# Performance work log

Measured on AMD Instinct MI355X. Metric: run time of the kernel, lower is better.

## Reference

```python
import jax, jax.numpy as jnp
import numpy as np

N_NODES = 10000
N_EDGES = 80000
OBS_DIMS = 128
HIDDEN = 1024
ACT_DIMS = 8
N_GRAPHS = 64


def setup_inputs() -> dict:
    key = jax.random.key(0)
    ks = jax.random.split(key, 8)
    x = jax.random.normal(ks[0], (N_NODES, OBS_DIMS), dtype=jnp.float32)
    edge_index = jax.random.randint(ks[1], (2, N_EDGES), 0, N_NODES, dtype=jnp.int64)
    batch = jnp.sort(jax.random.randint(ks[2], (N_NODES,), 0, N_GRAPHS, dtype=jnp.int64))
    # Glorot-style init for weights, zero bias (as in PyG GCNConv / Linear defaults)
    W1 = jax.random.normal(ks[3], (OBS_DIMS, HIDDEN), dtype=jnp.float32) * (1.0 / np.sqrt(OBS_DIMS))
    b1 = jnp.zeros((HIDDEN,), dtype=jnp.float32)
    W2 = jax.random.normal(ks[4], (HIDDEN, HIDDEN), dtype=jnp.float32) * (1.0 / np.sqrt(HIDDEN))
    b2 = jnp.zeros((HIDDEN,), dtype=jnp.float32)
    Wl = jax.random.normal(ks[5], (HIDDEN, ACT_DIMS), dtype=jnp.float32) * (1.0 / np.sqrt(HIDDEN))
    bl = jnp.zeros((ACT_DIMS,), dtype=jnp.float32)
    return {"x": x, "edge_index": edge_index, "batch": batch,
            "W1": W1, "b1": b1, "W2": W2, "b2": b2, "Wl": Wl, "bl": bl}


def _gcn_conv(x, src, dst, dinv, W, b, n):
    """PyG GCNConv: D^-1/2 (A+I) D^-1/2 X W + b (self-loops already in src/dst)."""
    h = x @ W                                   # [N, out]
    norm = (dinv[src] * dinv[dst])[:, None]      # [E+N, 1]
    msg = h[src] * norm                          # gather + scale
    out = jax.ops.segment_sum(msg, dst, num_segments=n)
    return out + b


def reference(x, edge_index, batch, W1, b1, W2, b2, Wl, bl):
    n = x.shape[0]
    loops = jnp.arange(n, dtype=edge_index.dtype)
    src = jnp.concatenate([edge_index[0], loops])  # add self-loops
    dst = jnp.concatenate([edge_index[1], loops])
    # degree (with self-loops) from destination column, as PyG does
    deg = jax.ops.segment_sum(jnp.ones_like(dst, dtype=x.dtype), dst, num_segments=n)
    dinv = jax.lax.rsqrt(jnp.maximum(deg, 1.0))

    h = jax.nn.relu(_gcn_conv(x, src, dst, dinv, W1, b1, n))
    h = _gcn_conv(h, src, dst, dinv, W2, b2, n)
    h = jnp.tanh(h @ Wl + bl)                    # [N, act_dims]

    # global_mean_pool over batch segment ids
    sums = jax.ops.segment_sum(h, batch, num_segments=N_GRAPHS)
    counts = jax.ops.segment_sum(jnp.ones((n, 1), h.dtype), batch, num_segments=N_GRAPHS)
    return sums / jnp.maximum(counts, 1.0)       # [N_GRAPHS, act_dims]
```

## Files before the change

kernel.cpp:

```cpp
#include <hip/hip_runtime.h>
#include <hip/hip_bf16.h>

#define NNODES 10000
#define NEDGES 80000
#define OBS    128
#define HID    1024
#define ACTD   8
#define NGR    64

typedef __bf16 bf16x8 __attribute__((ext_vector_type(8)));
typedef float  f32x4  __attribute__((ext_vector_type(4)));
typedef const __attribute__((address_space(1))) unsigned int gl_u32;
typedef __attribute__((address_space(3))) unsigned int lds_u32;

__device__ __forceinline__ ushort f2b(float f) {
    union { float f; unsigned int i; } v; v.f = f;
    unsigned int lsb = (v.i >> 16) & 1u;
    unsigned int r = v.i + 0x7fffu + lsb;
    return (ushort)(r >> 16);
}
__device__ __forceinline__ int cix(int v, int hi) {
    return v < 0 ? 0 : (v >= hi ? hi - 1 : v);
}

__global__ __launch_bounds__(256) void k_prep(const float* __restrict__ W1,
                                              const float* __restrict__ W2,
                                              const float* __restrict__ Wl,
                                              const float* __restrict__ b2,
                                              const float* __restrict__ bl,
                                              ushort* __restrict__ Wt1,
                                              ushort* __restrict__ M2bf,
                                              float* __restrict__ b2l,
                                              float* __restrict__ zacc,
                                              float* __restrict__ pool,
                                              float* __restrict__ cnt,
                                              int* __restrict__ ticket,
                                              int* __restrict__ degi) {
    int blk = blockIdx.x;
    if (blk >= 385) {
        int idx = (blk - 385) * 256 + threadIdx.x;
        if (idx < NNODES * ACTD) zacc[idx] = 0.0f;
        if (idx < NGR * ACTD) pool[idx] = 0.0f;
        if (idx < NGR) cnt[idx] = 0.0f;
        if (idx < NNODES) degi[idx] = 0;
        if (idx == 0) *ticket = 0;
        return;
    }
    if (blk < 128) {
        __shared__ float tile[32][33];
        int bx = (blk & 31) * 32, by = (blk >> 5) * 32;
        int tx = threadIdx.x & 31, ty = threadIdx.x >> 5;
        #pragma unroll
        for (int i = 0; i < 32; i += 8)
            tile[ty + i][tx] = W1[(size_t)(by + ty + i) * HID + bx + tx];
        __syncthreads();
        #pragma unroll
        for (int i = 0; i < 32; i += 8)
            Wt1[(size_t)(bx + ty + i) * OBS + by + tx] = f2b(tile[tx][ty + i]);
        return;
    }
    int wvid = ((blk - 128) * 256 + (int)threadIdx.x) >> 6;
    int lane = threadIdx.x & 63;
    if (wvid > HID) return;
    const float* row = (wvid == HID) ? b2 : (W2 + (size_t)wvid * HID);
    float acc[ACTD];
    #pragma unroll
    for (int j = 0; j < ACTD; ++j) acc[j] = 0.0f;
    for (int it = 0; it < HID / 64; ++it) {
        int k = it * 64 + lane;
        float w2v = row[k];
        float4 a = *(const float4*)(Wl + (size_t)k * ACTD);
        float4 b = *(const float4*)(Wl + (size_t)k * ACTD + 4);
        acc[0] += w2v * a.x; acc[1] += w2v * a.y; acc[2] += w2v * a.z; acc[3] += w2v * a.w;
        acc[4] += w2v * b.x; acc[5] += w2v * b.y; acc[6] += w2v * b.z; acc[7] += w2v * b.w;
    }
    #pragma unroll
    for (int off = 32; off > 0; off >>= 1)
        #pragma unroll
        for (int j = 0; j < ACTD; ++j)
            acc[j] += __shfl_down(acc[j], off);
    if (lane == 0) {
        if (wvid == HID) {
            #pragma unroll
            for (int j = 0; j < ACTD; ++j) b2l[j] = acc[j] + bl[j];
        } else {
            #pragma unroll
            for (int j = 0; j < ACTD; ++j) M2bf[wvid * ACTD + j] = f2b(acc[j]);
        }
    }
}

__global__ void k_count(const int* __restrict__ dst, int* degi, int e) {
    int i = blockIdx.x * 256 + threadIdx.x;
    if (i < e) atomicAdd(&degi[cix(dst[i], NNODES)], 1);
}

__global__ __launch_bounds__(1024) void k_scan(const int* __restrict__ degi,
                                               int* rowptr, int* cursor, float* dinv) {
    __shared__ int wsum[16];
    int t = threadIdx.x, lane = t & 63, w = t >> 6;
    int base = t * 10;
    int local[10];
    int s = 0;
    #pragma unroll
    for (int k = 0; k < 10; ++k) {
        int i = base + k;
        int v = 0;
        if (i < NNODES) {
            v = degi[i];
            dinv[i] = rsqrtf((float)(v + 1));
        }
        local[k] = s; s += v;
    }
    int sc = s;
    #pragma unroll
    for (int off = 1; off < 64; off <<= 1) {
        int u = __shfl_up(sc, off);
        if (lane >= off) sc += u;
    }
    if (lane == 63) wsum[w] = sc;
    __syncthreads();
    if (w == 0 && lane < 16) {
        int v = wsum[lane];
        #pragma unroll
        for (int off = 1; off < 16; off <<= 1) {
            int u = __shfl_up(v, off);
            if (lane >= off) v += u;
        }
        wsum[lane] = v;
    }
    __syncthreads();
    int excl = ((w == 0) ? 0 : wsum[w - 1]) + (sc - s);
    #pragma unroll
    for (int k = 0; k < 10; ++k) {
        int i = base + k;
        if (i < NNODES) { rowptr[i] = excl + local[k]; cursor[i] = excl + local[k]; }
    }
    if (t == 0) rowptr[NNODES] = wsum[15];
}

__global__ void k_fill(const int* __restrict__ src, const int* __restrict__ dst,
                       const float* __restrict__ dinv, int* cursor,
                       int2* __restrict__ epair, int e) {
    int i = blockIdx.x * 256 + threadIdx.x;
    if (i >= e) return;
    int s = cix(src[i], NNODES), d = cix(dst[i], NNODES);
    int pos = atomicAdd(&cursor[d], 1);
    epair[pos] = make_int2(s, __float_as_int(dinv[s] * dinv[d]));
}

__global__ void k_aggx(const float* __restrict__ x, const float* __restrict__ dinv,
                       const int* __restrict__ rowptr, const int2* __restrict__ epair,
                       ushort* __restrict__ aggbf, int n) {
    int wv = (blockIdx.x * 256 + threadIdx.x) >> 6;
    int lane = threadIdx.x & 63;
    if (wv >= n) return;
    int half = lane >> 5, li = lane & 31;
    float acc0 = 0.f, acc1 = 0.f, acc2 = 0.f, acc3 = 0.f;
    if (half == 0) {
        float d = dinv[wv], d2 = d * d;
        float4 sv = *((const float4*)(x + (size_t)wv * OBS) + li);
        acc0 = sv.x * d2; acc1 = sv.y * d2; acc2 = sv.z * d2; acc3 = sv.w * d2;
    }
    int e1 = rowptr[wv + 1];
    int e = rowptr[wv] + half;
    for (; e + 2 < e1; e += 4) {
        int2 p0 = epair[e], p1 = epair[e + 2];
        float c0 = __int_as_float(p0.y), c1 = __int_as_float(p1.y);
        float4 a = *((const float4*)(x + (size_t)p0.x * OBS) + li);
        float4 b = *((const float4*)(x + (size_t)p1.x * OBS) + li);
        acc0 += a.x * c0 + b.x * c1;
        acc1 += a.y * c0 + b.y * c1;
        acc2 += a.z * c0 + b.z * c1;
        acc3 += a.w * c0 + b.w * c1;
    }
    if (e < e1) {
        int2 p0 = epair[e];
        float c0 = __int_as_float(p0.y);
        float4 a = *((const float4*)(x + (size_t)p0.x * OBS) + li);
        acc0 += a.x * c0; acc1 += a.y * c0; acc2 += a.z * c0; acc3 += a.w * c0;
    }
    acc0 += __shfl_down(acc0, 32);
    acc1 += __shfl_down(acc1, 32);
    acc2 += __shfl_down(acc2, 32);
    acc3 += __shfl_down(acc3, 32);
    if (half == 0) {
        ushort4 o; o.x = f2b(acc0); o.y = f2b(acc1); o.z = f2b(acc2); o.w = f2b(acc3);
        *((ushort4*)(aggbf + (size_t)wv * OBS) + li) = o;
    }
}

__global__ __launch_bounds__(256) void k_gemm1_fused(const ushort* __restrict__ A,
                                                     const ushort* __restrict__ Bt,
                                                     const float* __restrict__ bias,
                                                     const ushort* __restrict__ M2bf,
                                                     float* __restrict__ zacc,
                                                     int M) {
    __shared__ ushort buf[128 * 136 + 16 * 128];
    ushort* As    = buf;
    ushort* Bs    = buf + 8192;
    ushort* stage = buf;
    ushort* M2t   = buf + 128 * 136;

    const int t = threadIdx.x;
    const int bm = blockIdx.x, bn = blockIdx.y;
    const int lane = t & 63, wv = t >> 6;
    const int wm = (wv & 1) * 64, wn = (wv >> 1) * 64;
    const int l16 = lane & 15, kg = (lane >> 4) * 8;

    if (t < 128) {
        ushort4 a = *(const ushort4*)(M2bf + (size_t)(bn * 128 + t) * ACTD);
        ushort4 b = *(const ushort4*)(M2bf + (size_t)(bn * 128 + t) * ACTD + 4);
        M2t[0 * 128 + t] = a.x; M2t[1 * 128 + t] = a.y;
        M2t[2 * 128 + t] = a.z; M2t[3 * 128 + t] = a.w;
        M2t[4 * 128 + t] = b.x; M2t[5 * 128 + t] = b.y;
        M2t[6 * 128 + t] = b.z; M2t[7 * 128 + t] = b.w;
        #pragma unroll
        for (int j = 8; j < 16; ++j) M2t[j * 128 + t] = 0;
    }

    f32x4 acc[4][4];
    #pragma unroll
    for (int i = 0; i < 4; ++i)
        #pragma unroll
        for (int j = 0; j < 4; ++j)
            acc[i][j] = (f32x4){0.f, 0.f, 0.f, 0.f};

    const int rs = t >> 3;
    const int cs = (t & 7) * 8;
    #pragma unroll
    for (int kt = 0; kt < OBS; kt += 64) {
        #pragma unroll
        for (int p = 0; p < 4; ++p) {
            int r = rs + p * 32;
            int gr = bm * 128 + r; if (gr >= M) gr = M - 1;
            __builtin_amdgcn_global_load_lds(
                (gl_u32*)(A + (size_t)gr * OBS + kt + cs),
                (lds_u32*)(As + r * 64 + cs), 16, 0, 0);
            int gn = bn * 128 + r;
            __builtin_amdgcn_global_load_lds(
                (gl_u32*)(Bt + (size_t)gn * OBS + kt + cs),
                (lds_u32*)(Bs + r * 64 + cs), 16, 0, 0);
        }
        __syncthreads();
        #pragma unroll
        for (int k2 = 0; k2 < 64; k2 += 32) {
            bf16x8 af[4], bfr[4];
            #pragma unroll
            for (int i = 0; i < 4; ++i)
                af[i] = *(const bf16x8*)(As + (wm + i * 16 + l16) * 64 + k2 + kg);
            #pragma unroll
            for (int j = 0; j < 4; ++j)
                bfr[j] = *(const bf16x8*)(Bs + (wn + j * 16 + l16) * 64 + k2 + kg);
            #pragma unroll
            for (int i = 0; i < 4; ++i)
                #pragma unroll
                for (int j = 0; j < 4; ++j)
                    acc[i][j] = __builtin_amdgcn_mfma_f32_16x16x32_bf16(af[i], bfr[j], acc[i][j], 0, 0, 0);
        }
        __syncthreads();
    }

    #pragma unroll
    for (int i = 0; i < 4; ++i) {
        int rowb = wm + i * 16 + (lane >> 4) * 4;
        #pragma unroll
        for (int j = 0; j < 4; ++j) {
            int col = wn + j * 16 + l16;
            float bj = bias[bn * 128 + col];
            #pragma unroll
            for (int r = 0; r < 4; ++r)
                stage[(rowb + r) * 136 + col] = f2b(fmaxf(acc[i][j][r] + bj, 0.0f));
        }
    }
    __syncthreads();

    #pragma unroll
    for (int st = 0; st < 2; ++st) {
        int row0 = wv * 32 + st * 16;
        f32x4 z = (f32x4){0.f, 0.f, 0.f, 0.f};
        #pragma unroll
        for (int kt = 0; kt < 128; kt += 32) {
            bf16x8 a = *(const bf16x8*)(stage + (row0 + l16) * 136 + kt + kg);
            bf16x8 b = *(const bf16x8*)(M2t + l16 * 128 + kt + kg);
            z = __builtin_amdgcn_mfma_f32_16x16x32_bf16(a, b, z, 0, 0, 0);
        }
        if (l16 < ACTD) {
            int rowb = bm * 128 + row0 + (lane >> 4) * 4;
            #pragma unroll
            for (int r = 0; r < 4; ++r)
                if (rowb + r < M)
                    atomicAdd(&zacc[(size_t)(rowb + r) * ACTD + l16], z[r]);
        }
    }
}

__global__ __launch_bounds__(1024) void k_zfinal(const float* __restrict__ zacc,
                                                 const float* __restrict__ dinv,
                                                 const int* __restrict__ rowptr,
                                                 const int2* __restrict__ epair,
                                                 const float* __restrict__ b2l,
                                                 const int* __restrict__ batch,
                                                 float* __restrict__ pool,
                                                 float* __restrict__ cnt,
                                                 int* __restrict__ ticket,
                                                 float* __restrict__ out, int n) {
    __shared__ float part[NGR * ACTD];
    __shared__ int   partc[NGR];
    __shared__ int   lastflag;
    int t = threadIdx.x;
    if (t < NGR * ACTD) part[t] = 0.0f;
    if (t < NGR) partc[t] = 0;
    __syncthreads();

    int idx = blockIdx.x * 1024 + t;
    int i = idx >> 3, j = idx & 7;
    if (i < n) {
        float d = dinv[i];
        float v = zacc[idx] * d * d;
        int e0 = rowptr[i], e1 = rowptr[i + 1];
        for (int e = e0; e < e1; ++e) {
            int2 p = epair[e];
            v += __int_as_float(p.y) * zacc[(size_t)p.x * ACTD + j];
        }
        float tz = tanhf(v + b2l[j]);
        int g = cix(batch[i], NGR);
        atomicAdd(&part[g * ACTD + j], tz);
        if (j == 0) atomicAdd(&partc[g], 1);
    }
    __syncthreads();

    int i0 = (blockIdx.x * 1024) >> 3;
    int i1 = (blockIdx.x * 1024 + 1023) >> 3;
    if (i0 < n) {
        if (i1 >= n) i1 = n - 1;
        int g0 = cix(batch[i0], NGR), g1 = cix(batch[i1], NGR);
        int ng = g1 - g0 + 1;
        if (t < ng * ACTD)
            atomicAdd(&pool[g0 * ACTD + t], part[g0 * ACTD + t]);
        if (t < ng) {
            int c = partc[g0 + t];
            if (c) atomicAdd(&cnt[g0 + t], (float)c);
        }
    }
    __syncthreads();
    if (t == 0) {
        __threadfence();
        int old = atomicAdd(ticket, 1);
        lastflag = (old == (int)gridDim.x - 1);
    }
    __syncthreads();
    if (lastflag && t < NGR * ACTD) {
        float pv = atomicAdd(&pool[t], 0.0f);
        float cv = atomicAdd(&cnt[t >> 3], 0.0f);
        out[t] = pv / fmaxf(cv, 1.0f);
    }
}

extern "C" void kernel_launch(void* const* d_in, const int* in_sizes, int n_in,
                              void* d_out, int out_size, void* d_ws, size_t ws_size,
                              hipStream_t stream) {
    const float* x   = (const float*)d_in[0];
    const int*   ei  = (const int*)d_in[1];
    const int*   bat = (const int*)d_in[2];
    const float* W1  = (const float*)d_in[3];
    const float* b1  = (const float*)d_in[4];
    const float* W2  = (const float*)d_in[5];
    const float* b2v = (const float*)d_in[6];
    const float* Wl  = (const float*)d_in[7];
    const float* bl  = (const float*)d_in[8];
    float* out = (float*)d_out;

    const int N = NNODES, E = NEDGES;
    const int* src = ei;
    const int* dst = ei + E;

    char* ws = (char*)d_ws;
    size_t off = 0;
    float*  pool   = (float*)(ws + off); off += 2048;
    float*  cnt    = (float*)(ws + off); off += 256;
    int*    ticket = (int*)(ws + off);   off += 256;
    float*  dinv   = (float*)(ws + off); off += 40192;
    int*    degi   = (int*)(ws + off);   off += 40192;
    int*    rowptr = (int*)(ws + off);   off += 40448;
    int*    cursor = (int*)(ws + off);   off += 40192;
    int2*   epair  = (int2*)(ws + off);  off += (size_t)E * 8;
    float*  b2l    = (float*)(ws + off); off += 256;
    ushort* M2bf   = (ushort*)(ws + off); off += (size_t)HID * ACTD * 2;
    ushort* Wt1    = (ushort*)(ws + off); off += (size_t)HID * OBS * 2;
    float*  zacc   = (float*)(ws + off); off += (size_t)N * ACTD * 4;
    ushort* aggbf  = (ushort*)(ws + off); off += (size_t)N * OBS * 2;

    k_prep<<<698, 256, 0, stream>>>(W1, W2, Wl, b2v, bl, Wt1, M2bf, b2l,
                                    zacc, pool, cnt, ticket, degi);
    k_count<<<(E + 255) / 256, 256, 0, stream>>>(dst, degi, E);
    k_scan<<<1, 1024, 0, stream>>>(degi, rowptr, cursor, dinv);
    k_fill<<<(E + 255) / 256, 256, 0, stream>>>(src, dst, dinv, cursor, epair, E);

    k_aggx<<<(N * 64 + 255) / 256, 256, 0, stream>>>(x, dinv, rowptr, epair, aggbf, N);

    k_gemm1_fused<<<dim3((N + 127) / 128, HID / 128), 256, 0, stream>>>(
        aggbf, Wt1, b1, M2bf, zacc, N);

    k_zfinal<<<(N * ACTD + 1023) / 1024, 1024, 0, stream>>>(
        zacc, dinv, rowptr, epair, b2l, bat, pool, cnt, ticket, out, N);
}
```

Baseline: 138.3 us.

## Gather bf16 copy of x in aggregation and fold degree count into prep

```diff
diff --git a/kernel.cpp b/kernel.cpp
--- a/kernel.cpp
+++ b/kernel.cpp
@@ -19,6 +19,9 @@
     unsigned int r = v.i + 0x7fffu + lsb;
     return (ushort)(r >> 16);
 }
+__device__ __forceinline__ float b2f(ushort u) {
+    union { unsigned int i; float f; } v; v.i = ((unsigned int)u) << 16; return v.f;
+}
 __device__ __forceinline__ int cix(int v, int hi) {
     return v < 0 ? 0 : (v >= hi ? hi - 1 : v);
 }
@@ -28,22 +31,29 @@
                                               const float* __restrict__ Wl,
                                               const float* __restrict__ b2,
                                               const float* __restrict__ bl,
+                                              const float* __restrict__ x,
+                                              const int* __restrict__ dst,
                                               ushort* __restrict__ Wt1,
                                               ushort* __restrict__ M2bf,
                                               float* __restrict__ b2l,
-                                              float* __restrict__ zacc,
-                                              float* __restrict__ pool,
-                                              float* __restrict__ cnt,
-                                              int* __restrict__ ticket,
-                                              int* __restrict__ degi) {
+                                              int* __restrict__ degi,
+                                              ushort* __restrict__ xbf) {
     int blk = blockIdx.x;
+    if (blk >= 449) {
+        int idx = (blk - 449) * 256 + threadIdx.x;
+        const float4* p = (const float4*)x + (size_t)idx * 2;
+        float4 a = p[0], b = p[1];
+        uint4 o;
+        o.x = (unsigned)f2b(a.x) | ((unsigned)f2b(a.y) << 16);
+        o.y = (unsigned)f2b(a.z) | ((unsigned)f2b(a.w) << 16);
+        o.z = (unsigned)f2b(b.x) | ((unsigned)f2b(b.y) << 16);
+        o.w = (unsigned)f2b(b.z) | ((unsigned)f2b(b.w) << 16);
+        *((uint4*)xbf + idx) = o;
+        return;
+    }
     if (blk >= 385) {
-        int idx = (blk - 385) * 256 + threadIdx.x;
-        if (idx < NNODES * ACTD) zacc[idx] = 0.0f;
-        if (idx < NGR * ACTD) pool[idx] = 0.0f;
-        if (idx < NGR) cnt[idx] = 0.0f;
-        if (idx < NNODES) degi[idx] = 0;
-        if (idx == 0) *ticket = 0;
+        for (int i = (blk - 385) * 256 + threadIdx.x; i < NEDGES; i += 64 * 256)
+            atomicAdd(&degi[cix(dst[i], NNODES)], 1);
         return;
     }
     if (blk < 128) {
@@ -90,11 +100,6 @@
     }
 }
 
-__global__ void k_count(const int* __restrict__ dst, int* degi, int e) {
-    int i = blockIdx.x * 256 + threadIdx.x;
-    if (i < e) atomicAdd(&degi[cix(dst[i], NNODES)], 1);
-}
-
 __global__ __launch_bounds__(1024) void k_scan(const int* __restrict__ degi,
                                                int* rowptr, int* cursor, float* dinv) {
     __shared__ int wsum[16];
@@ -149,7 +154,8 @@
     epair[pos] = make_int2(s, __float_as_int(dinv[s] * dinv[d]));
 }
 
-__global__ void k_aggx(const float* __restrict__ x, const float* __restrict__ dinv,
+__global__ void k_aggx(const float* __restrict__ x, const ushort* __restrict__ xbf,
+                       const float* __restrict__ dinv,
                        const int* __restrict__ rowptr, const int2* __restrict__ epair,
                        ushort* __restrict__ aggbf, int n) {
     int wv = (blockIdx.x * 256 + threadIdx.x) >> 6;
@@ -167,18 +173,19 @@
     for (; e + 2 < e1; e += 4) {
         int2 p0 = epair[e], p1 = epair[e + 2];
         float c0 = __int_as_float(p0.y), c1 = __int_as_float(p1.y);
-        float4 a = *((const float4*)(x + (size_t)p0.x * OBS) + li);
-        float4 b = *((const float4*)(x + (size_t)p1.x * OBS) + li);
-        acc0 += a.x * c0 + b.x * c1;
-        acc1 += a.y * c0 + b.y * c1;
-        acc2 += a.z * c0 + b.z * c1;
-        acc3 += a.w * c0 + b.w * c1;
+        ushort4 a = *((const ushort4*)(xbf + (size_t)p0.x * OBS) + li);
+        ushort4 b = *((const ushort4*)(xbf + (size_t)p1.x * OBS) + li);
+        acc0 += b2f(a.x) * c0 + b2f(b.x) * c1;
+        acc1 += b2f(a.y) * c0 + b2f(b.y) * c1;
+        acc2 += b2f(a.z) * c0 + b2f(b.z) * c1;
+        acc3 += b2f(a.w) * c0 + b2f(b.w) * c1;
     }
     if (e < e1) {
         int2 p0 = epair[e];
         float c0 = __int_as_float(p0.y);
-        float4 a = *((const float4*)(x + (size_t)p0.x * OBS) + li);
-        acc0 += a.x * c0; acc1 += a.y * c0; acc2 += a.z * c0; acc3 += a.w * c0;
+        ushort4 a = *((const ushort4*)(xbf + (size_t)p0.x * OBS) + li);
+        acc0 += b2f(a.x) * c0; acc1 += b2f(a.y) * c0;
+        acc2 += b2f(a.z) * c0; acc3 += b2f(a.w) * c0;
     }
     acc0 += __shfl_down(acc0, 32);
     acc1 += __shfl_down(acc1, 32);
@@ -380,24 +387,28 @@
     float*  pool   = (float*)(ws + off); off += 2048;
     float*  cnt    = (float*)(ws + off); off += 256;
     int*    ticket = (int*)(ws + off);   off += 256;
+    float*  zacc   = (float*)(ws + off); off += (size_t)N * ACTD * 4;
+    int*    degi   = (int*)(ws + off);   off += 40192;
+    const size_t ZEROSZ = off;
     float*  dinv   = (float*)(ws + off); off += 40192;
-    int*    degi   = (int*)(ws + off);   off += 40192;
     int*    rowptr = (int*)(ws + off);   off += 40448;
     int*    cursor = (int*)(ws + off);   off += 40192;
     int2*   epair  = (int2*)(ws + off);  off += (size_t)E * 8;
     float*  b2l    = (float*)(ws + off); off += 256;
     ushort* M2bf   = (ushort*)(ws + off); off += (size_t)HID * ACTD * 2;
     ushort* Wt1    = (ushort*)(ws + off); off += (size_t)HID * OBS * 2;
-    float*  zacc   = (float*)(ws + off); off += (size_t)N * ACTD * 4;
+    ushort* xbf    = (ushort*)(ws + off); off += (size_t)N * OBS * 2;
     ushort* aggbf  = (ushort*)(ws + off); off += (size_t)N * OBS * 2;
 
-    k_prep<<<698, 256, 0, stream>>>(W1, W2, Wl, b2v, bl, Wt1, M2bf, b2l,
-                                    zacc, pool, cnt, ticket, degi);
-    k_count<<<(E + 255) / 256, 256, 0, stream>>>(dst, degi, E);
+    hipMemsetAsync(d_ws, 0, ZEROSZ, stream);
+
+    k_prep<<<449 + (N * OBS / 8 + 255) / 256, 256, 0, stream>>>(
+        W1, W2, Wl, b2v, bl, x, dst, Wt1, M2bf, b2l, degi, xbf);
+
     k_scan<<<1, 1024, 0, stream>>>(degi, rowptr, cursor, dinv);
     k_fill<<<(E + 255) / 256, 256, 0, stream>>>(src, dst, dinv, cursor, epair, E);
 
-    k_aggx<<<(N * 64 + 255) / 256, 256, 0, stream>>>(x, dinv, rowptr, epair, aggbf, N);
+    k_aggx<<<(N * 64 + 255) / 256, 256, 0, stream>>>(x, xbf, dinv, rowptr, epair, aggbf, N);
 
     k_gemm1_fused<<<dim3((N + 127) / 128, HID / 128), 256, 0, stream>>>(
         aggbf, Wt1, b1, M2bf, zacc, N);
```

New measurement: 136.6 us. No clear change (-1.2%).
